# Performance work log

Hardware: AMD Instinct MI355X
Metric: run time of the kernel (lower is better)

## Reference

```python
import jax, jax.numpy as jnp
import numpy as np

N = 50000   # nodes
E = 600000  # edges
D = 128     # in = hidden = out channels
L = 3       # num_layers
LN_EPS = 1e-5


def setup_inputs() -> dict:
    key = jax.random.key(0)
    ks = jax.random.split(key, 4)
    x = jax.random.normal(ks[0], (N, D), dtype=jnp.float32)
    edge_index = jax.random.randint(ks[1], (2, E), 0, N, dtype=jnp.int32)
    # GCNConv linear weights (glorot-ish scale) and biases, one per layer
    Ws = jax.random.normal(ks[2], (L, D, D), dtype=jnp.float32) / np.sqrt(D)
    bs = jnp.zeros((L, D), dtype=jnp.float32)
    # LayerNorm affine params per layer
    ln_w = jnp.ones((L, D), dtype=jnp.float32)
    ln_b = jnp.zeros((L, D), dtype=jnp.float32)
    # PReLU (single shared slope per layer, torch default init 0.25)
    alphas = jnp.full((L,), 0.25, dtype=jnp.float32)
    return {"x": x, "edge_index": edge_index, "Ws": Ws, "bs": bs,
            "ln_w": ln_w, "ln_b": ln_b, "alphas": alphas}


def reference(x, edge_index, Ws, bs, ln_w, ln_b, alphas):
    # --- gcn_norm: add self-loops, symmetric D^{-1/2} (A+I) D^{-1/2} ---
    loop = jnp.arange(N, dtype=edge_index.dtype)
    src = jnp.concatenate([edge_index[0], loop])  # [E+N]
    dst = jnp.concatenate([edge_index[1], loop])  # [E+N]
    deg = jax.ops.segment_sum(jnp.ones_like(dst, dtype=x.dtype), dst,
                              num_segments=N)
    dinv = jnp.where(deg > 0, jax.lax.rsqrt(jnp.maximum(deg, 1.0)), 0.0)
    norm = (dinv[src] * dinv[dst])[:, None]  # [E+N, 1]

    h = x
    for l in range(L):
        # GCNConv: linear -> gather -> scale -> scatter-add -> bias
        h = h @ Ws[l]                                   # [N, D]
        msg = h[src] * norm                             # [E+N, D]
        h = jax.ops.segment_sum(msg, dst, num_segments=N) + bs[l]
        # LayerNorm over feature dim
        mu = jnp.mean(h, axis=-1, keepdims=True)
        var = jnp.mean((h - mu) ** 2, axis=-1, keepdims=True)
        h = (h - mu) * jax.lax.rsqrt(var + LN_EPS) * ln_w[l] + ln_b[l]
        # PReLU
        h = jnp.where(h >= 0, h, alphas[l] * h)
    return h
```

## Files before the change

kernel.cpp:

```cpp
#include <hip/hip_runtime.h>
#include <hip/hip_bf16.h>

#define NN 50000
#define EE 600000
#define DD 128
#define LL 3
#define LN_EPS 1e-5f
#define CAP 64
#define ALD 136

typedef __attribute__((ext_vector_type(8))) short short8;
typedef __attribute__((ext_vector_type(4))) float floatx4;

__device__ inline unsigned short f2bf(float f) {
    union { float f; unsigned u; } a; a.f = f;
    unsigned r = a.u + 0x7fffu + ((a.u >> 16) & 1u);
    return (unsigned short)(r >> 16);
}


__global__ __launch_bounds__(256) void init_kernel(const float* __restrict__ W,
                                                   unsigned short* __restrict__ Wt,
                                                   int* __restrict__ cnt) {
    for (int i = blockIdx.x * 256 + threadIdx.x; i < NN; i += gridDim.x * 256)
        cnt[i] = 0;
    for (int i = blockIdx.x * 256 + threadIdx.x; i < LL * DD * DD; i += gridDim.x * 256) {
        int l = i >> 14, n = (i >> 7) & 127, k = i & 127;
        Wt[i] = f2bf(W[(l << 14) + k * DD + n]);
    }
}


__global__ void fill_kernel(const int* __restrict__ src, const int* __restrict__ dst,
                            int* __restrict__ cnt, int* __restrict__ csrc) {
    int i = blockIdx.x * blockDim.x + threadIdx.x;
    if (i >= EE) return;
    int d = dst[i];
    int pos = atomicAdd(&cnt[d], 1);
    csrc[(size_t)d * CAP + pos] = src[i];
}


__global__ __launch_bounds__(256) void gemm0_kernel(const float* __restrict__ A,
                                                    const unsigned short* __restrict__ Wt,
                                                    const int* __restrict__ cnt,
                                                    unsigned short* __restrict__ Cb) {
    __shared__ unsigned short alds[32 * ALD];
    int tid = threadIdx.x;
    int lane = tid & 63;
    int w = tid >> 6;
    int rowbase = blockIdx.x * 32;

    int cbase = (w & 1) * 64;
    int nIdx = cbase + (lane & 15);
    int kq = (lane >> 4) * 8;

    {
        int r = tid >> 3;
        int k0 = (tid & 7) * 16;
        int grow = rowbase + r;
        unsigned short* dstp = &alds[r * ALD + k0];
        if (grow < NN) {
            const float* ap = &A[(size_t)grow * DD + k0];
            float4 v0 = *(const float4*)&ap[0];
            float4 v1 = *(const float4*)&ap[4];
            float4 v2 = *(const float4*)&ap[8];
            float4 v3 = *(const float4*)&ap[12];
            float fv[16] = {v0.x,v0.y,v0.z,v0.w, v1.x,v1.y,v1.z,v1.w,
                            v2.x,v2.y,v2.z,v2.w, v3.x,v3.y,v3.z,v3.w};
            unsigned short uv[16];
            #pragma unroll
            for (int q = 0; q < 16; q++) uv[q] = f2bf(fv[q]);
            *(uint4*)&dstp[0] = *(uint4*)&uv[0];
            *(uint4*)&dstp[8] = *(uint4*)&uv[8];
        } else {
            uint4 z = make_uint4(0, 0, 0, 0);
            *(uint4*)&dstp[0] = z;
            *(uint4*)&dstp[8] = z;
        }
    }
    __syncthreads();

    int rbase = (w >> 1) * 16;
    int mrow = rbase + (lane & 15);
    floatx4 acc[4] = {{0.f,0.f,0.f,0.f},{0.f,0.f,0.f,0.f},
                      {0.f,0.f,0.f,0.f},{0.f,0.f,0.f,0.f}};
    #pragma unroll
    for (int t = 0; t < 4; t++) {
        short8 a = *(const short8*)&alds[mrow * ALD + t * 32 + kq];
        #pragma unroll
        for (int j = 0; j < 4; j++) {
            short8 b = *(const short8*)&Wt[(nIdx + j * 16) * DD + t * 32 + kq];
            acc[j] = __builtin_amdgcn_mfma_f32_16x16x32_bf16(a, b, acc[j], 0, 0, 0);
        }
    }

    int gnode0 = rowbase + rbase + (lane >> 4) * 4;
    #pragma unroll
    for (int i = 0; i < 4; i++) {
        int node = gnode0 + i;
        if (node < NN) {
            float dv = rsqrtf((float)(cnt[node] + 1));
            #pragma unroll
            for (int j = 0; j < 4; j++)
                Cb[(size_t)node * DD + cbase + j * 16 + (lane & 15)] = f2bf(acc[j][i] * dv);
        }
    }
}


__device__ inline void acc_row(float* acc, uint4 t) {
    unsigned uu[4] = {t.x, t.y, t.z, t.w};
    #pragma unroll
    for (int q = 0; q < 4; q++) {
        union { unsigned x; float f; } lo, hi;
        lo.x = uu[q] << 16;
        hi.x = uu[q] & 0xffff0000u;
        acc[2 * q]     += lo.f;
        acc[2 * q + 1] += hi.f;
    }
}

__device__ inline void agg_node(const unsigned short* __restrict__ Tb,
                                const int* __restrict__ cnt, const int* __restrict__ csrc,
                                const float* bv, const float* wv, const float* cv,
                                float alpha, int node, int f8, float* yv) {
    int deg = cnt[node];
    float dv = rsqrtf((float)(deg + 1));
    const int* row = &csrc[(size_t)node * CAP];

    float acc[8] = {};
    acc_row(acc, *(const uint4*)&Tb[(size_t)node * DD + f8]);

    int k = 0;
    for (; k + 4 <= deg; k += 4) {
        int4 ss = *(const int4*)&row[k];
        uint4 t0 = *(const uint4*)&Tb[(size_t)ss.x * DD + f8];
        uint4 t1 = *(const uint4*)&Tb[(size_t)ss.y * DD + f8];
        uint4 t2 = *(const uint4*)&Tb[(size_t)ss.z * DD + f8];
        uint4 t3 = *(const uint4*)&Tb[(size_t)ss.w * DD + f8];
        acc_row(acc, t0); acc_row(acc, t1); acc_row(acc, t2); acc_row(acc, t3);
    }
    for (; k < deg; k++) {
        acc_row(acc, *(const uint4*)&Tb[(size_t)row[k] * DD + f8]);
    }

    float a[8];
    float s1 = 0.f, s2 = 0.f;
    #pragma unroll
    for (int q = 0; q < 8; q++) {
        a[q] = fmaf(acc[q], dv, bv[q]);
        s1 += a[q]; s2 += a[q] * a[q];
    }
    #pragma unroll
    for (int off = 8; off > 0; off >>= 1) {
        s1 += __shfl_xor(s1, off, 16);
        s2 += __shfl_xor(s2, off, 16);
    }
    float mu = s1 * (1.f / DD);
    float var = s2 * (1.f / DD) - mu * mu;
    float rstd = rsqrtf(var + LN_EPS);
    #pragma unroll
    for (int q = 0; q < 8; q++) {
        float y = (a[q] - mu) * rstd * wv[q] + cv[q];
        yv[q] = (y >= 0.f) ? y : alpha * y;
    }
}


__global__ __launch_bounds__(256) void aggemm_kernel(
    const unsigned short* __restrict__ Tb, const int* __restrict__ cnt,
    const int* __restrict__ csrc,
    const float* __restrict__ bias, const float* __restrict__ lnw,
    const float* __restrict__ lnb, const float* __restrict__ alphas, int layer,
    const unsigned short* __restrict__ Wt, unsigned short* __restrict__ Tout) {
    __shared__ unsigned short alds[32 * ALD];
    int tid = threadIdx.x;
    int g = tid >> 4;
    int lane16 = tid & 15;
    int f8 = lane16 * 8;
    int nodebase = blockIdx.x * 32;

    float4 b0 = *(const float4*)&bias[f8];
    float4 b1 = *(const float4*)&bias[f8 + 4];
    float4 w0 = *(const float4*)&lnw[f8];
    float4 w1 = *(const float4*)&lnw[f8 + 4];
    float4 c0 = *(const float4*)&lnb[f8];
    float4 c1 = *(const float4*)&lnb[f8 + 4];
    float bv[8] = {b0.x, b0.y, b0.z, b0.w, b1.x, b1.y, b1.z, b1.w};
    float wv[8] = {w0.x, w0.y, w0.z, w0.w, w1.x, w1.y, w1.z, w1.w};
    float cv[8] = {c0.x, c0.y, c0.z, c0.w, c1.x, c1.y, c1.z, c1.w};
    float alpha = alphas[layer];

    #pragma unroll
    for (int j = 0; j < 2; j++) {
        int r = j * 16 + g;
        int node = nodebase + r;
        unsigned short* dstp = &alds[r * ALD + f8];
        if (node < NN) {
            float yv[8];
            agg_node(Tb, cnt, csrc, bv, wv, cv, alpha, node, f8, yv);
            unsigned short pv[8];
            #pragma unroll
            for (int q = 0; q < 8; q++) pv[q] = f2bf(yv[q]);
            *(uint4*)dstp = *(uint4*)&pv[0];
        } else {
            *(uint4*)dstp = make_uint4(0, 0, 0, 0);
        }
    }
    __syncthreads();

    int lane = tid & 63;
    int w = tid >> 6;
    int cbase = (w & 1) * 64;
    int nIdx = cbase + (lane & 15);
    int kq = (lane >> 4) * 8;
    int rbase = (w >> 1) * 16;
    int mrow = rbase + (lane & 15);
    floatx4 acc[4] = {{0.f,0.f,0.f,0.f},{0.f,0.f,0.f,0.f},
                      {0.f,0.f,0.f,0.f},{0.f,0.f,0.f,0.f}};
    #pragma unroll
    for (int t = 0; t < 4; t++) {
        short8 a = *(const short8*)&alds[mrow * ALD + t * 32 + kq];
        #pragma unroll
        for (int jj = 0; jj < 4; jj++) {
            short8 b = *(const short8*)&Wt[(nIdx + jj * 16) * DD + t * 32 + kq];
            acc[jj] = __builtin_amdgcn_mfma_f32_16x16x32_bf16(a, b, acc[jj], 0, 0, 0);
        }
    }
    int gnode0 = nodebase + rbase + (lane >> 4) * 4;
    #pragma unroll
    for (int i = 0; i < 4; i++) {
        int node = gnode0 + i;
        if (node < NN) {
            float dv = rsqrtf((float)(cnt[node] + 1));
            #pragma unroll
            for (int jj = 0; jj < 4; jj++)
                Tout[(size_t)node * DD + cbase + jj * 16 + (lane & 15)] = f2bf(acc[jj][i] * dv);
        }
    }
}


__global__ __launch_bounds__(256) void agg_final_kernel(
    const unsigned short* __restrict__ Tb, const int* __restrict__ cnt,
    const int* __restrict__ csrc,
    const float* __restrict__ bias, const float* __restrict__ lnw,
    const float* __restrict__ lnb, const float* __restrict__ alphas, int layer,
    float* __restrict__ out) {
    int g = threadIdx.x >> 4;
    int lane16 = threadIdx.x & 15;
    int f8 = lane16 * 8;
    int node = blockIdx.x * 16 + g;
    if (node >= NN) return;

    float4 b0 = *(const float4*)&bias[f8];
    float4 b1 = *(const float4*)&bias[f8 + 4];
    float4 w0 = *(const float4*)&lnw[f8];
    float4 w1 = *(const float4*)&lnw[f8 + 4];
    float4 c0 = *(const float4*)&lnb[f8];
    float4 c1 = *(const float4*)&lnb[f8 + 4];
    float bv[8] = {b0.x, b0.y, b0.z, b0.w, b1.x, b1.y, b1.z, b1.w};
    float wv[8] = {w0.x, w0.y, w0.z, w0.w, w1.x, w1.y, w1.z, w1.w};
    float cv[8] = {c0.x, c0.y, c0.z, c0.w, c1.x, c1.y, c1.z, c1.w};

    float yv[8];
    agg_node(Tb, cnt, csrc, bv, wv, cv, alphas[layer], node, f8, yv);

    float* op = &out[(size_t)node * DD + f8];
    *(float4*)&op[0] = make_float4(yv[0], yv[1], yv[2], yv[3]);
    *(float4*)&op[4] = make_float4(yv[4], yv[5], yv[6], yv[7]);
}


extern "C" void kernel_launch(void* const* d_in, const int* in_sizes, int n_in,
                              void* d_out, int out_size, void* d_ws, size_t ws_size,
                              hipStream_t stream) {
    const float* x    = (const float*)d_in[0];
    const int*   ei   = (const int*)d_in[1];
    const float* Ws   = (const float*)d_in[2];
    const float* bs   = (const float*)d_in[3];
    const float* lnw  = (const float*)d_in[4];
    const float* lnb  = (const float*)d_in[5];
    const float* alphas = (const float*)d_in[6];
    float* out = (float*)d_out;

    const int* src = ei;
    const int* dst = ei + EE;

    char* ws = (char*)d_ws;
    size_t off = 0;
    auto alloc = [&](size_t bytes) -> void* {
        void* p = ws + off;
        off = (off + bytes + 255) & ~(size_t)255;
        return p;
    };
    int* cnt  = (int*)alloc(NN * sizeof(int));
    int* csrc = (int*)alloc((size_t)NN * CAP * sizeof(int));
    unsigned short* wt    = (unsigned short*)alloc((size_t)LL * DD * DD * sizeof(unsigned short));
    unsigned short* tbufA = (unsigned short*)alloc((size_t)NN * DD * sizeof(unsigned short));
    unsigned short* tbufB = (unsigned short*)alloc((size_t)NN * DD * sizeof(unsigned short));

    init_kernel<<<256, 256, 0, stream>>>(Ws, wt, cnt);
    fill_kernel<<<(EE + 255) / 256, 256, 0, stream>>>(src, dst, cnt, csrc);

    const int tile_grid = (NN + 31) / 32;
    gemm0_kernel<<<tile_grid, 256, 0, stream>>>(x, wt, cnt, tbufA);
    aggemm_kernel<<<tile_grid, 256, 0, stream>>>(tbufA, cnt, csrc,
                                                 bs + 0 * DD, lnw + 0 * DD, lnb + 0 * DD,
                                                 alphas, 0, wt + 1 * DD * DD, tbufB);
    aggemm_kernel<<<tile_grid, 256, 0, stream>>>(tbufB, cnt, csrc,
                                                 bs + 1 * DD, lnw + 1 * DD, lnb + 1 * DD,
                                                 alphas, 1, wt + 2 * DD * DD, tbufA);
    agg_final_kernel<<<(NN + 15) / 16, 256, 0, stream>>>(tbufA, cnt, csrc,
                                                         bs + 2 * DD, lnw + 2 * DD, lnb + 2 * DD,
                                                         alphas, 2, out);
}
```

Before: 256.4 us.

## Dynamically schedule node aggregation in larger 128-node tiles and fuse init into fill

The fused aggregate+GEMM kernel now handles 128 nodes per block with 512 threads. Each 16-lane group pulls its next node from a shared-memory atomic counter, so uneven node degrees spread across groups instead of fixing two nodes per group. Each wave then computes a full 16x128 output tile with eight MFMA accumulators, and the weight transpose is folded into the edge-fill kernel, with a memset replacing the counter-zeroing init. The trade-off is fewer, larger blocks (about 391 over the GPU's CUs), which may leave a partial last wave of blocks, plus more accumulator registers per wave.

Result: no change. 254.7 us (-0.7%).

```diff
diff --git a/kernel.cpp b/kernel.cpp
--- a/kernel.cpp
+++ b/kernel.cpp
@@ -8,6 +8,7 @@
 #define LN_EPS 1e-5f
 #define CAP 64
 #define ALD 136
+#define POOL 128
 
 typedef __attribute__((ext_vector_type(8))) short short8;
 typedef __attribute__((ext_vector_type(4))) float floatx4;
@@ -19,21 +20,14 @@
 }
 
 
-__global__ __launch_bounds__(256) void init_kernel(const float* __restrict__ W,
-                                                   unsigned short* __restrict__ Wt,
-                                                   int* __restrict__ cnt) {
-    for (int i = blockIdx.x * 256 + threadIdx.x; i < NN; i += gridDim.x * 256)
-        cnt[i] = 0;
-    for (int i = blockIdx.x * 256 + threadIdx.x; i < LL * DD * DD; i += gridDim.x * 256) {
+__global__ void fill_kernel(const int* __restrict__ src, const int* __restrict__ dst,
+                            const float* __restrict__ W, unsigned short* __restrict__ Wt,
+                            int* __restrict__ cnt, int* __restrict__ csrc) {
+    int i = blockIdx.x * blockDim.x + threadIdx.x;
+    if (i < LL * DD * DD) {
         int l = i >> 14, n = (i >> 7) & 127, k = i & 127;
         Wt[i] = f2bf(W[(l << 14) + k * DD + n]);
     }
-}
-
-
-__global__ void fill_kernel(const int* __restrict__ src, const int* __restrict__ dst,
-                            int* __restrict__ cnt, int* __restrict__ csrc) {
-    int i = blockIdx.x * blockDim.x + threadIdx.x;
     if (i >= EE) return;
     int d = dst[i];
     int pos = atomicAdd(&cnt[d], 1);
@@ -168,18 +162,19 @@
 }
 
 
-__global__ __launch_bounds__(256) void aggemm_kernel(
+__global__ __launch_bounds__(512) void aggemm_kernel(
     const unsigned short* __restrict__ Tb, const int* __restrict__ cnt,
     const int* __restrict__ csrc,
     const float* __restrict__ bias, const float* __restrict__ lnw,
     const float* __restrict__ lnb, const float* __restrict__ alphas, int layer,
     const unsigned short* __restrict__ Wt, unsigned short* __restrict__ Tout) {
-    __shared__ unsigned short alds[32 * ALD];
+    __shared__ unsigned short alds[POOL * ALD];
+    __shared__ int nextslot;
     int tid = threadIdx.x;
-    int g = tid >> 4;
     int lane16 = tid & 15;
     int f8 = lane16 * 8;
-    int nodebase = blockIdx.x * 32;
+    int nodebase = blockIdx.x * POOL;
+    if (tid == 0) nextslot = 0;
 
     float4 b0 = *(const float4*)&bias[f8];
     float4 b1 = *(const float4*)&bias[f8 + 4];
@@ -191,12 +186,15 @@
     float wv[8] = {w0.x, w0.y, w0.z, w0.w, w1.x, w1.y, w1.z, w1.w};
     float cv[8] = {c0.x, c0.y, c0.z, c0.w, c1.x, c1.y, c1.z, c1.w};
     float alpha = alphas[layer];
-
-    #pragma unroll
-    for (int j = 0; j < 2; j++) {
-        int r = j * 16 + g;
-        int node = nodebase + r;
-        unsigned short* dstp = &alds[r * ALD + f8];
+    __syncthreads();
+
+    for (;;) {
+        int sv = 0;
+        if (lane16 == 0) sv = atomicAdd(&nextslot, 1);
+        int s = __shfl(sv, 0, 16);
+        if (s >= POOL) break;
+        int node = nodebase + s;
+        unsigned short* dstp = &alds[s * ALD + f8];
         if (node < NN) {
             float yv[8];
             agg_node(Tb, cnt, csrc, bv, wv, cv, alpha, node, f8, yv);
@@ -212,20 +210,20 @@
 
     int lane = tid & 63;
     int w = tid >> 6;
-    int cbase = (w & 1) * 64;
-    int nIdx = cbase + (lane & 15);
+    int rbase = w * 16;
     int kq = (lane >> 4) * 8;
-    int rbase = (w >> 1) * 16;
     int mrow = rbase + (lane & 15);
-    floatx4 acc[4] = {{0.f,0.f,0.f,0.f},{0.f,0.f,0.f,0.f},
+    int nIdx = lane & 15;
+    floatx4 acc[8] = {{0.f,0.f,0.f,0.f},{0.f,0.f,0.f,0.f},{0.f,0.f,0.f,0.f},
+                      {0.f,0.f,0.f,0.f},{0.f,0.f,0.f,0.f},{0.f,0.f,0.f,0.f},
                       {0.f,0.f,0.f,0.f},{0.f,0.f,0.f,0.f}};
     #pragma unroll
     for (int t = 0; t < 4; t++) {
         short8 a = *(const short8*)&alds[mrow * ALD + t * 32 + kq];
         #pragma unroll
-        for (int jj = 0; jj < 4; jj++) {
-            short8 b = *(const short8*)&Wt[(nIdx + jj * 16) * DD + t * 32 + kq];
-            acc[jj] = __builtin_amdgcn_mfma_f32_16x16x32_bf16(a, b, acc[jj], 0, 0, 0);
+        for (int j = 0; j < 8; j++) {
+            short8 b = *(const short8*)&Wt[(nIdx + j * 16) * DD + t * 32 + kq];
+            acc[j] = __builtin_amdgcn_mfma_f32_16x16x32_bf16(a, b, acc[j], 0, 0, 0);
         }
     }
     int gnode0 = nodebase + rbase + (lane >> 4) * 4;
@@ -235,8 +233,8 @@
         if (node < NN) {
             float dv = rsqrtf((float)(cnt[node] + 1));
             #pragma unroll
-            for (int jj = 0; jj < 4; jj++)
-                Tout[(size_t)node * DD + cbase + jj * 16 + (lane & 15)] = f2bf(acc[jj][i] * dv);
+            for (int j = 0; j < 8; j++)
+                Tout[(size_t)node * DD + j * 16 + (lane & 15)] = f2bf(acc[j][i] * dv);
         }
     }
 }
@@ -301,17 +299,18 @@
     unsigned short* tbufA = (unsigned short*)alloc((size_t)NN * DD * sizeof(unsigned short));
     unsigned short* tbufB = (unsigned short*)alloc((size_t)NN * DD * sizeof(unsigned short));
 
-    init_kernel<<<256, 256, 0, stream>>>(Ws, wt, cnt);
-    fill_kernel<<<(EE + 255) / 256, 256, 0, stream>>>(src, dst, cnt, csrc);
-
-    const int tile_grid = (NN + 31) / 32;
-    gemm0_kernel<<<tile_grid, 256, 0, stream>>>(x, wt, cnt, tbufA);
-    aggemm_kernel<<<tile_grid, 256, 0, stream>>>(tbufA, cnt, csrc,
-                                                 bs + 0 * DD, lnw + 0 * DD, lnb + 0 * DD,
-                                                 alphas, 0, wt + 1 * DD * DD, tbufB);
-    aggemm_kernel<<<tile_grid, 256, 0, stream>>>(tbufB, cnt, csrc,
-                                                 bs + 1 * DD, lnw + 1 * DD, lnb + 1 * DD,
-                                                 alphas, 1, wt + 2 * DD * DD, tbufA);
+    hipMemsetAsync(cnt, 0, NN * sizeof(int), stream);
+    fill_kernel<<<(EE + 255) / 256, 256, 0, stream>>>(src, dst, Ws, wt, cnt, csrc);
+
+    gemm0_kernel<<<(NN + 31) / 32, 256, 0, stream>>>(x, wt, cnt, tbufA);
+
+    const int agg_grid = (NN + POOL - 1) / POOL;
+    aggemm_kernel<<<agg_grid, 512, 0, stream>>>(tbufA, cnt, csrc,
+                                                bs + 0 * DD, lnw + 0 * DD, lnb + 0 * DD,
+                                                alphas, 0, wt + 1 * DD * DD, tbufB);
+    aggemm_kernel<<<agg_grid, 512, 0, stream>>>(tbufB, cnt, csrc,
+                                                bs + 1 * DD, lnw + 1 * DD, lnb + 1 * DD,
+                                                alphas, 1, wt + 2 * DD * DD, tbufA);
     agg_final_kernel<<<(NN + 15) / 16, 256, 0, stream>>>(tbufA, cnt, csrc,
                                                          bs + 2 * DD, lnw + 2 * DD, lnb + 2 * DD,
                                                          alphas, 2, out);
```
